# Optimization experiments

Hardware: AMD Instinct MI355X
Metric: run time of the kernel (lower is better)

The kernel has to match this reference:

```python
import jax, jax.numpy as jnp
import numpy as np

B, D, H, C = 8192, 2048, 4096, 64
HALF = D // 2
BLOCKS = 2


def setup_inputs() -> dict:
    key = jax.random.key(0)
    ks = jax.random.split(key, 8)
    z = jax.random.normal(ks[0], (B, D), jnp.float32)
    condition = jax.random.normal(ks[1], (B, C), jnp.float32)
    # alternating masks: block 0 identity=odd indices, transform=even; block 1 flipped
    even = jnp.arange(0, D, 2, dtype=jnp.int32)
    odd = jnp.arange(1, D, 2, dtype=jnp.int32)
    idx_id = jnp.stack([odd, even])   # [BLOCKS, HALF]
    idx_tr = jnp.stack([even, odd])   # [BLOCKS, HALF]
    def init_w(k, shape, fan_in):
        return jax.random.normal(k, shape, jnp.float32) * np.float32(1.0 / np.sqrt(fan_in))
    W1 = init_w(ks[2], (BLOCKS, HALF + C, H), HALF + C)
    b1 = jnp.zeros((BLOCKS, H), jnp.float32)
    W2 = init_w(ks[3], (BLOCKS, H, H), H)
    b2 = jnp.zeros((BLOCKS, H), jnp.float32)
    W3 = init_w(ks[4], (BLOCKS, H, 2 * HALF), H) * np.float32(0.01)  # keep exp(S) tame
    b3 = jnp.zeros((BLOCKS, 2 * HALF), jnp.float32)
    return {"z": z, "condition": condition, "idx_id": idx_id, "idx_tr": idx_tr,
            "W1": W1, "b1": b1, "W2": W2, "b2": b2, "W3": W3, "b3": b3}


def reference(z, condition, idx_id, idx_tr, W1, b1, W2, b2, W3, b3):
    # F_zx of the affine coupling layer (scale_tanh=False, clamp_scale=None)
    x = z
    log_det = jnp.zeros((z.shape[0], 1), z.dtype)
    for i in range(BLOCKS):
        # gather identity channels, condition on external vector
        h = jnp.concatenate([x[:, idx_id[i]], condition], axis=-1)  # [B, HALF+C]
        h = jax.nn.relu(h @ W1[i] + b1[i])
        h = jax.nn.relu(h @ W2[i] + b2[i])
        out = (h @ W3[i] + b3[i]).reshape(x.shape[0], HALF, 2)
        S = out[..., 0]  # scale logits
        T = out[..., 1]  # translation
        # scatter-update transformed channels
        x = x.at[:, idx_tr[i]].set(x[:, idx_tr[i]] * jnp.exp(S) + T)
        log_det = log_det + jnp.sum(S, axis=1, keepdims=True)
    return x, log_det
```

## Files before the change

kernel.cpp:

```cpp
#include <hip/hip_runtime.h>
#include <hip/hip_bf16.h>

#define B_    8192
#define D_    2048
#define H_    4096
#define C_    64
#define HALF_ 1024
#define KIN_  1088

typedef __attribute__((ext_vector_type(8))) short bf16x8;
typedef __attribute__((ext_vector_type(4))) float f32x4;

__device__ __forceinline__ unsigned short f2bf(float f) {
  __hip_bfloat16 h = __float2bfloat16(f);
  return *reinterpret_cast<unsigned short*>(&h);
}

__device__ __forceinline__ void gload16(const void* g, void* s) {
  __builtin_amdgcn_global_load_lds((const __attribute__((address_space(1))) void*)g,
                                   (__attribute__((address_space(3))) void*)s,
                                   16, 0, 0);
}

__global__ void convT(const float* __restrict__ W, unsigned short* __restrict__ Wt,
                      int K, int N) {
  __shared__ float tile[32][33];
  int tx = threadIdx.x & 31, ty = threadIdx.x >> 5;
  int n0 = blockIdx.x * 32, k0 = blockIdx.y * 32;
#pragma unroll
  for (int i = 0; i < 4; ++i)
    tile[ty + i * 8][tx] = W[(size_t)(k0 + ty + i * 8) * N + n0 + tx];
  __syncthreads();
#pragma unroll
  for (int i = 0; i < 4; ++i)
    Wt[(size_t)(n0 + ty + i * 8) * K + k0 + tx] = f2bf(tile[tx][ty + i * 8]);
}

__global__ void build_act(const float* __restrict__ xsrc, const float* __restrict__ cond,
                          int par, unsigned short* __restrict__ A0) {
  int row = blockIdx.y;
  int col = blockIdx.x * 256 + threadIdx.x;
  if (col >= KIN_) return;
  float v;
  if (col < HALF_) {
    float2 p = ((const float2*)xsrc)[(size_t)row * (D_ / 2) + col];
    v = par ? p.y : p.x;
  } else {
    v = cond[(size_t)row * C_ + (col - HALF_)];
  }
  A0[(size_t)row * KIN_ + col] = f2bf(v);
}

template <int MODE>
__global__ __launch_bounds__(512, 2)
void gemm8p(const unsigned short* __restrict__ A,
            const unsigned short* __restrict__ Bt,
            const float* __restrict__ bias,
            unsigned short* __restrict__ Cout,
            const float* __restrict__ xold, float* __restrict__ xnew,
            float* __restrict__ part, int par,
            int M, int N, int K) {
  __shared__ unsigned short lds[65536];
  char* ldsb = (char*)lds;
  const int tid = threadIdx.x;
  const int w = tid >> 6, lane = tid & 63;
  const int fr = lane & 15, fq = lane >> 4;
  const int wr = w >> 2, wc = w & 3;

  const int nbx = N >> 8;
  const int nwg = (int)gridDim.x;
  const int cpx = nwg >> 3;
  const int bid = (int)blockIdx.x;
  const int swz = (bid & 7) * cpx + (bid >> 3);
  const int by = swz / nbx, bx = swz - by * nbx;
  const int m0 = by << 8, n0 = bx << 8;

  const int chunkp = (((fr & 1) << 2) | fq) ^ (fr >> 1);
  const int A0 = (wr * 64 + (fr >> 1)) * 128 + chunkp * 16;
  const int B0 = 32768 + (wc * 32 + (fr >> 1)) * 128 + chunkp * 16;

  int rS[2], kcolS[2];
#pragma unroll
  for (int s = 0; s < 2; ++s) {
    int q = s * 512 + w * 64 + lane;
    int p = q >> 3, cph = q & 7;
    int clg = cph ^ (p & 7);
    rS[s] = 2 * p + (clg >> 2);
    kcolS[s] = (clg & 3) * 8;
  }
  const unsigned short* sA0 = A + (size_t)(m0 + rS[0]) * K + kcolS[0];
  const unsigned short* sA1 = A + (size_t)(m0 + rS[1]) * K + kcolS[1];
  const unsigned short* sB0 = Bt + (size_t)(n0 + rS[0]) * K + kcolS[0];
  const unsigned short* sB1 = Bt + (size_t)(n0 + rS[1]) * K + kcolS[1];
  const int dst0 = w * 1024 + lane * 16;

#define STAGE_A(KK, TILE, BUF) do {                                          \
    gload16(sA0 + (TILE) * 64 + (KK) * 32,                                   \
            ldsb + (BUF) + (KK) * 16384 + dst0);                             \
    gload16(sA1 + (TILE) * 64 + (KK) * 32,                                   \
            ldsb + (BUF) + (KK) * 16384 + 8192 + dst0);                      \
  } while (0)
#define STAGE_B(KK, TILE, BUF) do {                                          \
    gload16(sB0 + (TILE) * 64 + (KK) * 32,                                   \
            ldsb + (BUF) + 32768 + (KK) * 16384 + dst0);                     \
    gload16(sB1 + (TILE) * 64 + (KK) * 32,                                   \
            ldsb + (BUF) + 32768 + (KK) * 16384 + 8192 + dst0);              \
  } while (0)

  f32x4 acc[8][4];
  f32x4 z4 = {0.f, 0.f, 0.f, 0.f};
#pragma unroll
  for (int m = 0; m < 8; ++m)
#pragma unroll
    for (int n = 0; n < 4; ++n) acc[m][n] = z4;

  const int NT = K >> 6;

  STAGE_A(0, 0, 0);
  STAGE_A(1, 0, 0);
  STAGE_B(0, 0, 0);
  STAGE_B(1, 0, 0);
  STAGE_B(0, 1, 65536);
  STAGE_A(0, 1, 65536);
  STAGE_B(1, 1, 65536);
  asm volatile("s_waitcnt vmcnt(6)" ::: "memory");
  __builtin_amdgcn_sched_barrier(0);
  __builtin_amdgcn_s_barrier();

#define MFMA16(MB)                                                           \
    __builtin_amdgcn_s_setprio(1);                                           \
    _Pragma("unroll") for (int m = 0; m < 4; ++m)                            \
      _Pragma("unroll") for (int n = 0; n < 4; ++n)                          \
        acc[(MB) + m][n] = __builtin_amdgcn_mfma_f32_16x16x32_bf16(          \
            av[m], bv[n], acc[(MB) + m][n], 0, 0, 0);                        \
    __builtin_amdgcn_s_setprio(0);

#define TILE8(TT, S1, S234, DO_VM)                                           \
  {                                                                          \
    const int bufC = ((TT) & 1) * 65536;                                     \
    const int bufN = 65536 - bufC;                                           \
    bf16x8 av[4], bv[4];                                                     \
                               \
    _Pragma("unroll") for (int m = 0; m < 4; ++m)                            \
      av[m] = *(const bf16x8*)(ldsb + bufC + A0 + m * 1024);                 \
    _Pragma("unroll") for (int n = 0; n < 4; ++n)                            \
      bv[n] = *(const bf16x8*)(ldsb + bufC + B0 + n * 1024);                 \
    if (S1) { STAGE_A(1, (TT) + 1, bufN); }                                  \
    __builtin_amdgcn_s_barrier();                                            \
    MFMA16(0)                                                                \
    __builtin_amdgcn_s_barrier();                                            \
                                 \
    _Pragma("unroll") for (int m = 0; m < 4; ++m)                            \
      av[m] = *(const bf16x8*)(ldsb + bufC + A0 + (m + 4) * 1024);           \
    if (S234) { STAGE_B(0, (TT) + 2, bufC); }                                \
    __builtin_amdgcn_s_barrier();                                            \
    MFMA16(4)                                                                \
    __builtin_amdgcn_s_barrier();                                            \
                               \
    _Pragma("unroll") for (int m = 0; m < 4; ++m)                            \
      av[m] = *(const bf16x8*)(ldsb + bufC + A0 + m * 1024 + 16384);         \
    _Pragma("unroll") for (int n = 0; n < 4; ++n)                            \
      bv[n] = *(const bf16x8*)(ldsb + bufC + B0 + n * 1024 + 16384);         \
    if (S234) { STAGE_A(0, (TT) + 2, bufC); }                                \
    __builtin_amdgcn_s_barrier();                                            \
    MFMA16(0)                                                                \
    __builtin_amdgcn_s_barrier();                                            \
                                           \
    _Pragma("unroll") for (int m = 0; m < 4; ++m)                            \
      av[m] = *(const bf16x8*)(ldsb + bufC + A0 + (m + 4) * 1024 + 16384);   \
    if (S234) { STAGE_B(1, (TT) + 2, bufC); }                                \
    __builtin_amdgcn_s_barrier();                                            \
    MFMA16(4)                                                                \
    if (DO_VM == 1) asm volatile("s_waitcnt vmcnt(6)" ::: "memory");         \
    if (DO_VM == 2) asm volatile("s_waitcnt vmcnt(0)" ::: "memory");         \
    __builtin_amdgcn_sched_barrier(0);                                       \
    __builtin_amdgcn_s_barrier();                                            \
  }

  for (int T = 0; T < NT - 2; ++T) {
    TILE8(T, 1, 1, 1)
  }
  TILE8(NT - 2, 1, 0, 2)
  TILE8(NT - 1, 0, 0, 0)
#undef TILE8
#undef MFMA16
#undef STAGE_A
#undef STAGE_B

  if (MODE == 0) {
#pragma unroll
    for (int m = 0; m < 8; ++m)
#pragma unroll
      for (int n = 0; n < 4; ++n) {
        int gcol = n0 + wc * 64 + n * 16 + fr;
        float bb = bias[gcol];
#pragma unroll
        for (int r = 0; r < 4; ++r) {
          float v = fmaxf(acc[m][n][r] + bb, 0.f);
          int lrow = m * 16 + fq * 4 + r;
          *(unsigned short*)(ldsb + w * 16384 + lrow * 128 + ((n ^ fq) * 32) + fr * 2) = f2bf(v);
        }
      }
    asm volatile("s_waitcnt lgkmcnt(0)" ::: "memory");
    __builtin_amdgcn_sched_barrier(0);
    unsigned short* Cb = Cout + (size_t)(m0 + wr * 128) * N + n0 + wc * 64;
    const int sub = lane & 7;
#pragma unroll
    for (int i = 0; i < 16; ++i) {
      int lrow = i * 8 + (lane >> 3);
      int phys = (sub >> 1) ^ ((lrow >> 2) & 3);
      bf16x8 val = *(const bf16x8*)(ldsb + w * 16384 + lrow * 128 + phys * 32 + (sub & 1) * 16);
      *(bf16x8*)(Cb + (size_t)lrow * N + sub * 8) = val;
    }
  } else {
#pragma unroll
    for (int m = 0; m < 8; ++m) {
      float srow[4] = {0.f, 0.f, 0.f, 0.f};
#pragma unroll
      for (int n = 0; n < 4; ++n) {
        int gcol = n0 + wc * 64 + n * 16 + fr;
        float bb = bias[gcol];
#pragma unroll
        for (int r = 0; r < 4; ++r) {
          float v = acc[m][n][r] + bb;
          float vp = __shfl_xor(v, 1);
          if (!(fr & 1)) {
            int grow = m0 + wr * 128 + m * 16 + fq * 4 + r;
            size_t idx = (size_t)grow * N + gcol + par;
            xnew[idx] = xold[idx] * expf(v) + vp;
            srow[r] += v;
          }
        }
      }
#pragma unroll
      for (int r = 0; r < 4; ++r) {
        float s = srow[r];
        s += __shfl_xor(s, 2);
        s += __shfl_xor(s, 4);
        s += __shfl_xor(s, 8);
        if (fr == 0) {
          int grow = m0 + wr * 128 + m * 16 + fq * 4 + r;
          part[(size_t)grow * 32 + bx * 4 + wc] = s;
        }
      }
    }
  }
}

__global__ void reduce_logdet(const float* __restrict__ P, float* __restrict__ logdet, int add) {
  int row = blockIdx.x * 256 + threadIdx.x;
  float s = 0.f;
#pragma unroll
  for (int g = 0; g < 32; ++g) s += P[(size_t)row * 32 + g];
  logdet[row] = add ? (logdet[row] + s) : s;
}

extern "C" void kernel_launch(void* const* d_in, const int* in_sizes, int n_in,
                              void* d_out, int out_size, void* d_ws, size_t ws_size,
                              hipStream_t stream) {
  const float* z    = (const float*)d_in[0];
  const float* cond = (const float*)d_in[1];
  const float* W1   = (const float*)d_in[4];
  const float* b1   = (const float*)d_in[5];
  const float* W2   = (const float*)d_in[6];
  const float* b2   = (const float*)d_in[7];
  const float* W3   = (const float*)d_in[8];
  const float* b3   = (const float*)d_in[9];

  float* xout   = (float*)d_out;
  float* logdet = xout + (size_t)B_ * D_;

  char* ws = (char*)d_ws;
  unsigned short* Wt = (unsigned short*)ws;
  unsigned short* H1 = (unsigned short*)(ws + 33554432);
  unsigned short* H2 = (unsigned short*)(ws + 33554432 + 67108864);
  float* Pp = (float*)H1;
  unsigned short* A0 = H2;

  for (int blk = 0; blk < 2; ++blk) {
    const float* W1b = W1 + (size_t)blk * KIN_ * H_;
    const float* W2b = W2 + (size_t)blk * H_ * H_;
    const float* W3b = W3 + (size_t)blk * H_ * D_;
    const float* b1b = b1 + (size_t)blk * H_;
    const float* b2b = b2 + (size_t)blk * H_;
    const float* b3b = b3 + (size_t)blk * D_;
    const float* xsrc = blk ? xout : z;

    convT<<<dim3(H_ / 32, KIN_ / 32), 256, 0, stream>>>(W1b, Wt, KIN_, H_);
    build_act<<<dim3(5, B_), 256, 0, stream>>>(xsrc, cond, 1 - blk, A0);
    gemm8p<0><<<dim3((H_ / 256) * (B_ / 256)), 512, 0, stream>>>(
        A0, Wt, b1b, H1, nullptr, nullptr, nullptr, 0, B_, H_, KIN_);

    convT<<<dim3(H_ / 32, H_ / 32), 256, 0, stream>>>(W2b, Wt, H_, H_);
    gemm8p<0><<<dim3((H_ / 256) * (B_ / 256)), 512, 0, stream>>>(
        H1, Wt, b2b, H2, nullptr, nullptr, nullptr, 0, B_, H_, H_);

    convT<<<dim3(D_ / 32, H_ / 32), 256, 0, stream>>>(W3b, Wt, H_, D_);
    gemm8p<1><<<dim3((D_ / 256) * (B_ / 256)), 512, 0, stream>>>(
        H2, Wt, b3b, nullptr, z, xout, Pp, blk, B_, D_, H_);

    reduce_logdet<<<dim3(B_ / 256), 256, 0, stream>>>(Pp, logdet, blk);
  }
}
```

Measured before the change: 1.035 ms.

## Prefetch LDS fragments into separate registers and halve barriers per K-tile

Restructures the inner GEMM tile loop so A/B fragments for the next MFMA group are loaded from LDS into distinct register sets ahead of the current MFMAs, rather than reusing a single av/bv set. Removes about half of the workgroup barriers per tile, letting LDS reads overlap matrix math. In exchange it uses more VGPRs, which may reduce occupancy, and the lighter barrier pattern must still keep the double-buffered LDS staging correctly ordered.

```diff
diff --git a/kernel.cpp b/kernel.cpp
--- a/kernel.cpp
+++ b/kernel.cpp
@@ -127,54 +127,53 @@
   __builtin_amdgcn_sched_barrier(0);
   __builtin_amdgcn_s_barrier();
 
-#define MFMA16(MB)                                                           \
+#define MFMA16(MB, AV, BV)                                                   \
     __builtin_amdgcn_s_setprio(1);                                           \
     _Pragma("unroll") for (int m = 0; m < 4; ++m)                            \
       _Pragma("unroll") for (int n = 0; n < 4; ++n)                          \
         acc[(MB) + m][n] = __builtin_amdgcn_mfma_f32_16x16x32_bf16(          \
-            av[m], bv[n], acc[(MB) + m][n], 0, 0, 0);                        \
+            AV[m], BV[n], acc[(MB) + m][n], 0, 0, 0);                        \
     __builtin_amdgcn_s_setprio(0);
 
 #define TILE8(TT, S1, S234, DO_VM)                                           \
   {                                                                          \
     const int bufC = ((TT) & 1) * 65536;                                     \
     const int bufN = 65536 - bufC;                                           \
-    bf16x8 av[4], bv[4];                                                     \
-                               \
-    _Pragma("unroll") for (int m = 0; m < 4; ++m)                            \
-      av[m] = *(const bf16x8*)(ldsb + bufC + A0 + m * 1024);                 \
+    bf16x8 bv0[4], a00[4], a01[4], bv1[4], a10[4], a11[4];                   \
+                                               \
     _Pragma("unroll") for (int n = 0; n < 4; ++n)                            \
-      bv[n] = *(const bf16x8*)(ldsb + bufC + B0 + n * 1024);                 \
+      bv0[n] = *(const bf16x8*)(ldsb + bufC + B0 + n * 1024);                \
+    _Pragma("unroll") for (int m = 0; m < 4; ++m)                            \
+      a00[m] = *(const bf16x8*)(ldsb + bufC + A0 + m * 1024);                \
+    _Pragma("unroll") for (int m = 0; m < 4; ++m)                            \
+      a01[m] = *(const bf16x8*)(ldsb + bufC + A0 + (m + 4) * 1024);          \
+    __builtin_amdgcn_sched_barrier(0);                                       \
     if (S1) { STAGE_A(1, (TT) + 1, bufN); }                                  \
-    __builtin_amdgcn_s_barrier();                                            \
-    MFMA16(0)                                                                \
-    __builtin_amdgcn_s_barrier();                                            \
-                                 \
-    _Pragma("unroll") for (int m = 0; m < 4; ++m)                            \
-      av[m] = *(const bf16x8*)(ldsb + bufC + A0 + (m + 4) * 1024);           \
+                        \
+    MFMA16(0, a00, bv0)                                                      \
+    __builtin_amdgcn_s_barrier();     \
+                         \
+    _Pragma("unroll") for (int n = 0; n < 4; ++n)                            \
+      bv1[n] = *(const bf16x8*)(ldsb + bufC + B0 + n * 1024 + 16384);        \
+    _Pragma("unroll") for (int m = 0; m < 4; ++m)                            \
+      a10[m] = *(const bf16x8*)(ldsb + bufC + A0 + m * 1024 + 16384);        \
+    __builtin_amdgcn_sched_barrier(0);                                       \
     if (S234) { STAGE_B(0, (TT) + 2, bufC); }                                \
-    __builtin_amdgcn_s_barrier();                                            \
-    MFMA16(4)                                                                \
-    __builtin_amdgcn_s_barrier();                                            \
-                               \
-    _Pragma("unroll") for (int m = 0; m < 4; ++m)                            \
-      av[m] = *(const bf16x8*)(ldsb + bufC + A0 + m * 1024 + 16384);         \
-    _Pragma("unroll") for (int n = 0; n < 4; ++n)                            \
-      bv[n] = *(const bf16x8*)(ldsb + bufC + B0 + n * 1024 + 16384);         \
+    MFMA16(4, a01, bv0)                                                      \
+    __builtin_amdgcn_s_barrier();                      \
+                         \
+    _Pragma("unroll") for (int m = 0; m < 4; ++m)                            \
+      a11[m] = *(const bf16x8*)(ldsb + bufC + A0 + (m + 4) * 1024 + 16384);  \
+    __builtin_amdgcn_sched_barrier(0);                                       \
     if (S234) { STAGE_A(0, (TT) + 2, bufC); }                                \
-    __builtin_amdgcn_s_barrier();                                            \
-    MFMA16(0)                                                                \
-    __builtin_amdgcn_s_barrier();                                            \
-                                           \
-    _Pragma("unroll") for (int m = 0; m < 4; ++m)                            \
-      av[m] = *(const bf16x8*)(ldsb + bufC + A0 + (m + 4) * 1024 + 16384);   \
+    MFMA16(0, a10, bv1)                                                      \
+    __builtin_amdgcn_s_barrier();                  \
     if (S234) { STAGE_B(1, (TT) + 2, bufC); }                                \
-    __builtin_amdgcn_s_barrier();                                            \
-    MFMA16(4)                                                                \
+    MFMA16(4, a11, bv1)                                                      \
     if (DO_VM == 1) asm volatile("s_waitcnt vmcnt(6)" ::: "memory");         \
     if (DO_VM == 2) asm volatile("s_waitcnt vmcnt(0)" ::: "memory");         \
     __builtin_amdgcn_sched_barrier(0);                                       \
-    __builtin_amdgcn_s_barrier();                                            \
+    __builtin_amdgcn_s_barrier();   \
   }
 
   for (int T = 0; T < NT - 2; ++T) {
```

New measurement: 1.024 ms. No clear change (-1.0%).

## Restructure GEMM main loop into triple-buffered K=32 windows with register double-buffering

Applied to the files above, without the earlier changes.

Replaces the 64-wide K tile, double-buffered LDS schedule with four barriers per tile by a 32-wide K step rotated through three LDS buffers. Each window issues all A/B global-to-LDS loads for a future step, waits with a single barrier, prefetches the next fragments into a second register set, and runs 32 MFMAs on the current set. The aim is fewer barriers and better overlap of LDS reads with MFMA. In exchange it roughly doubles fragment register usage and shortens the prefetch distance per step.

```diff
diff --git a/kernel.cpp b/kernel.cpp
--- a/kernel.cpp
+++ b/kernel.cpp
@@ -77,7 +77,7 @@
 
   const int chunkp = (((fr & 1) << 2) | fq) ^ (fr >> 1);
   const int A0 = (wr * 64 + (fr >> 1)) * 128 + chunkp * 16;
-  const int B0 = 32768 + (wc * 32 + (fr >> 1)) * 128 + chunkp * 16;
+  const int B0 = 16384 + (wc * 32 + (fr >> 1)) * 128 + chunkp * 16;
 
   int rS[2], kcolS[2];
 #pragma unroll
@@ -94,18 +94,39 @@
   const unsigned short* sB1 = Bt + (size_t)(n0 + rS[1]) * K + kcolS[1];
   const int dst0 = w * 1024 + lane * 16;
 
-#define STAGE_A(KK, TILE, BUF) do {                                          \
-    gload16(sA0 + (TILE) * 64 + (KK) * 32,                                   \
-            ldsb + (BUF) + (KK) * 16384 + dst0);                             \
-    gload16(sA1 + (TILE) * 64 + (KK) * 32,                                   \
-            ldsb + (BUF) + (KK) * 16384 + 8192 + dst0);                      \
+#define STAGE_ALL(OFF) do {                                                  \
+    gload16(sA0, ldsb + (OFF) + dst0);                                       \
+    gload16(sA1, ldsb + (OFF) + 8192 + dst0);                                \
+    gload16(sB0, ldsb + (OFF) + 16384 + dst0);                               \
+    gload16(sB1, ldsb + (OFF) + 24576 + dst0);                               \
+    sA0 += 32; sA1 += 32; sB0 += 32; sB1 += 32;                              \
   } while (0)
-#define STAGE_B(KK, TILE, BUF) do {                                          \
-    gload16(sB0 + (TILE) * 64 + (KK) * 32,                                   \
-            ldsb + (BUF) + 32768 + (KK) * 16384 + dst0);                     \
-    gload16(sB1 + (TILE) * 64 + (KK) * 32,                                   \
-            ldsb + (BUF) + 32768 + (KK) * 16384 + 8192 + dst0);              \
-  } while (0)
+
+#define RDFRAGS(AV, BV, OFF)                                                 \
+    _Pragma("unroll") for (int n = 0; n < 4; ++n)                            \
+      BV[n] = *(const bf16x8*)(ldsb + (OFF) + B0 + n * 1024);                \
+    _Pragma("unroll") for (int m = 0; m < 8; ++m)                            \
+      AV[m] = *(const bf16x8*)(ldsb + (OFF) + A0 + m * 1024);
+
+#define MFMA32(AV, BV)                                                       \
+    __builtin_amdgcn_s_setprio(1);                                           \
+    _Pragma("unroll") for (int m = 0; m < 8; ++m)                            \
+      _Pragma("unroll") for (int n = 0; n < 4; ++n)                          \
+        acc[m][n] = __builtin_amdgcn_mfma_f32_16x16x32_bf16(                 \
+            AV[m], BV[n], acc[m][n], 0, 0, 0);                               \
+    __builtin_amdgcn_s_setprio(0);
+
+#define WIN(STG, VM, RD, AVr, BVr, AVm, BVm)                                 \
+  {                                                                          \
+    if (STG) STAGE_ALL(stg);                                                 \
+    if (VM == 1) asm volatile("s_waitcnt vmcnt(4)" ::: "memory");            \
+    if (VM == 2) asm volatile("s_waitcnt vmcnt(0)" ::: "memory");            \
+    __builtin_amdgcn_sched_barrier(0);                                       \
+    __builtin_amdgcn_s_barrier();                                            \
+    if (RD) { RDFRAGS(AVr, BVr, nxt) }                                       \
+    MFMA32(AVm, BVm)                                                         \
+    int _t = cur; cur = nxt; nxt = stg; stg = _t;                            \
+  }
 
   f32x4 acc[8][4];
   f32x4 z4 = {0.f, 0.f, 0.f, 0.f};
@@ -114,78 +135,29 @@
 #pragma unroll
     for (int n = 0; n < 4; ++n) acc[m][n] = z4;
 
-  const int NT = K >> 6;
-
-  STAGE_A(0, 0, 0);
-  STAGE_A(1, 0, 0);
-  STAGE_B(0, 0, 0);
-  STAGE_B(1, 0, 0);
-  STAGE_B(0, 1, 65536);
-  STAGE_A(0, 1, 65536);
-  STAGE_B(1, 1, 65536);
-  asm volatile("s_waitcnt vmcnt(6)" ::: "memory");
+  const int NT = K >> 5;
+
+  bf16x8 av0[8], bv0[4], av1[8], bv1[4];
+
+  STAGE_ALL(0);
+  STAGE_ALL(32768);
+  asm volatile("s_waitcnt vmcnt(4)" ::: "memory");
   __builtin_amdgcn_sched_barrier(0);
   __builtin_amdgcn_s_barrier();
-
-#define MFMA16(MB)                                                           \
-    __builtin_amdgcn_s_setprio(1);                                           \
-    _Pragma("unroll") for (int m = 0; m < 4; ++m)                            \
-      _Pragma("unroll") for (int n = 0; n < 4; ++n)                          \
-        acc[(MB) + m][n] = __builtin_amdgcn_mfma_f32_16x16x32_bf16(          \
-            av[m], bv[n], acc[(MB) + m][n], 0, 0, 0);                        \
-    __builtin_amdgcn_s_setprio(0);
-
-#define TILE8(TT, S1, S234, DO_VM)                                           \
-  {                                                                          \
-    const int bufC = ((TT) & 1) * 65536;                                     \
-    const int bufN = 65536 - bufC;                                           \
-    bf16x8 av[4], bv[4];                                                     \
-                               \
-    _Pragma("unroll") for (int m = 0; m < 4; ++m)                            \
-      av[m] = *(const bf16x8*)(ldsb + bufC + A0 + m * 1024);                 \
-    _Pragma("unroll") for (int n = 0; n < 4; ++n)                            \
-      bv[n] = *(const bf16x8*)(ldsb + bufC + B0 + n * 1024);                 \
-    if (S1) { STAGE_A(1, (TT) + 1, bufN); }                                  \
-    __builtin_amdgcn_s_barrier();                                            \
-    MFMA16(0)                                                                \
-    __builtin_amdgcn_s_barrier();                                            \
-                                 \
-    _Pragma("unroll") for (int m = 0; m < 4; ++m)                            \
-      av[m] = *(const bf16x8*)(ldsb + bufC + A0 + (m + 4) * 1024);           \
-    if (S234) { STAGE_B(0, (TT) + 2, bufC); }                                \
-    __builtin_amdgcn_s_barrier();                                            \
-    MFMA16(4)                                                                \
-    __builtin_amdgcn_s_barrier();                                            \
-                               \
-    _Pragma("unroll") for (int m = 0; m < 4; ++m)                            \
-      av[m] = *(const bf16x8*)(ldsb + bufC + A0 + m * 1024 + 16384);         \
-    _Pragma("unroll") for (int n = 0; n < 4; ++n)                            \
-      bv[n] = *(const bf16x8*)(ldsb + bufC + B0 + n * 1024 + 16384);         \
-    if (S234) { STAGE_A(0, (TT) + 2, bufC); }                                \
-    __builtin_amdgcn_s_barrier();                                            \
-    MFMA16(0)                                                                \
-    __builtin_amdgcn_s_barrier();                                            \
-                                           \
-    _Pragma("unroll") for (int m = 0; m < 4; ++m)                            \
-      av[m] = *(const bf16x8*)(ldsb + bufC + A0 + (m + 4) * 1024 + 16384);   \
-    if (S234) { STAGE_B(1, (TT) + 2, bufC); }                                \
-    __builtin_amdgcn_s_barrier();                                            \
-    MFMA16(4)                                                                \
-    if (DO_VM == 1) asm volatile("s_waitcnt vmcnt(6)" ::: "memory");         \
-    if (DO_VM == 2) asm volatile("s_waitcnt vmcnt(0)" ::: "memory");         \
-    __builtin_amdgcn_sched_barrier(0);                                       \
-    __builtin_amdgcn_s_barrier();                                            \
-  }
-
-  for (int T = 0; T < NT - 2; ++T) {
-    TILE8(T, 1, 1, 1)
-  }
-  TILE8(NT - 2, 1, 0, 2)
-  TILE8(NT - 1, 0, 0, 0)
-#undef TILE8
-#undef MFMA16
-#undef STAGE_A
-#undef STAGE_B
+  RDFRAGS(av0, bv0, 0)
+  int cur = 0, nxt = 32768, stg = 65536;
+
+  for (int P = 0; P < (NT - 2) / 2; ++P) {
+    WIN(1, 1, 1, av1, bv1, av0, bv0)
+    WIN(1, 1, 1, av0, bv0, av1, bv1)
+  }
+  WIN(0, 2, 1, av1, bv1, av0, bv0)
+  WIN(0, 0, 0, av1, bv1, av1, bv1)
+  __builtin_amdgcn_s_barrier();
+#undef WIN
+#undef MFMA32
+#undef RDFRAGS
+#undef STAGE_ALL
 
   if (MODE == 0) {
 #pragma unroll
```

After: 1.022 ms. Within noise of the previous version (-1.3%).
